# Kernel tuning notes

Hardware: AMD Instinct MI355X
Metric: run time of the kernel (lower is better)

Reference implementation:

```python
import jax, jax.numpy as jnp
import numpy as np

N, L, E, H = 2, 2048, 1024, 16
D = E // H  # head_dimension


def setup_inputs() -> dict:
    key = jax.random.key(0)
    kq, kk, kv, km, kw, kb = jax.random.split(key, 6)
    return {
        "query": jax.random.normal(kq, (N, L, E), dtype=jnp.float32),
        "key": jax.random.normal(kk, (N, L, E), dtype=jnp.float32),
        "value": jax.random.normal(kv, (N, L, E), dtype=jnp.float32),
        "mask": jax.random.randint(km, (N, 1, L, L), 0, 2, dtype=jnp.int32),
        "W_out": jax.random.normal(kw, (E, E), dtype=jnp.float32) / np.float32(np.sqrt(E)),
        "b_out": jax.random.normal(kb, (E,), dtype=jnp.float32) * np.float32(0.02),
    }


def reference(query, key, value, mask, W_out, b_out):
    n, ql, e = query.shape
    # split heads: [N, L, E] -> [N, L, H, D]
    q = query.reshape(n, ql, H, D)
    k = key.reshape(n, key.shape[1], H, D)
    v = value.reshape(n, value.shape[1], H, D)
    # energy: [N, H, Q, K]
    energy = jnp.einsum('nqhd,nkhd->nhqk', q, k)
    energy = jnp.where(mask == 0, jnp.float32(-1e20), energy)
    scale = jnp.float32(E) ** jnp.float32(0.5)
    attention = jax.nn.softmax(energy / scale, axis=3)
    out = jnp.einsum('nhql,nlhd->nqhd', attention, v).reshape(n, ql, H * D)
    # fully_connected_output: torch Linear -> x @ W^T + b
    return out @ W_out.T + b_out
```

## Files before the change

kernel.cpp:

```cpp
#include <hip/hip_runtime.h>
#include <hip/hip_bf16.h>

#define N_ 2
#define L_ 2048
#define E_ 1024
#define H_ 16
#define D_ 64

typedef __attribute__((ext_vector_type(8))) short bf16x8;
typedef __attribute__((ext_vector_type(4))) short bf16x4;
typedef __attribute__((ext_vector_type(4))) float f32x4;

static __device__ __forceinline__ short bfc(float f) {
    union { __bf16 h; short s; } u;
    u.h = (__bf16)f;
    return u.s;
}

static __device__ __forceinline__ void glds16(const void* g, void* l) {
    __builtin_amdgcn_global_load_lds(
        (const __attribute__((address_space(1))) unsigned int*)g,
        (__attribute__((address_space(3))) unsigned int*)l, 16, 0, 0);
}

__global__ __launch_bounds__(256) void pack_kv(
    const float* __restrict__ K, const float* __restrict__ V,
    unsigned short* __restrict__ Kp, unsigned short* __restrict__ Vp)
{
    __shared__ short T[64][72];

    const int bx = blockIdx.x;
    const int kt = bx & 31;
    const int h  = (bx >> 5) & 15;
    const int n  = bx >> 9;
    const int tid = threadIdx.x;
    const int kq = tid >> 4, c4 = tid & 15;

    const size_t inbase = ((size_t)(n * L_) + kt * 64) * E_ + h * D_;
    const size_t obase  = ((size_t)((n * H_ + h) * 32 + kt)) * 4096;

#pragma unroll
    for (int jj = 0; jj < 4; ++jj) {
        const int r = kq + jj * 16;
        const float4 f = *reinterpret_cast<const float4*>(K + inbase + (size_t)r * E_ + c4 * 4);
        bf16x4 w;
        w[0] = bfc(f.x); w[1] = bfc(f.y); w[2] = bfc(f.z); w[3] = bfc(f.w);
        *reinterpret_cast<bf16x4*>(&Kp[obase + r * 64 + ((c4 * 4) ^ ((r & 7) << 3))]) = w;
    }
#pragma unroll
    for (int jj = 0; jj < 4; ++jj) {
        const int k = kq + jj * 16;
        const float4 f = *reinterpret_cast<const float4*>(V + inbase + (size_t)k * E_ + c4 * 4);
        T[c4 * 4 + 0][k] = bfc(f.x);
        T[c4 * 4 + 1][k] = bfc(f.y);
        T[c4 * 4 + 2][k] = bfc(f.z);
        T[c4 * 4 + 3][k] = bfc(f.w);
    }
    __syncthreads();
#pragma unroll
    for (int jj = 0; jj < 2; ++jj) {
        const int d  = (tid >> 3) + jj * 32;
        const int k8 = (tid & 7) * 8;
        const bf16x8 v = *reinterpret_cast<const bf16x8*>(&T[d][k8]);
        *reinterpret_cast<bf16x8*>(&Vp[obase + d * 64 + (k8 ^ ((d & 7) << 3))]) = v;
    }
}

__global__ __launch_bounds__(256) void pack_mask(
    const int* __restrict__ mask, unsigned long long* __restrict__ Mb)
{
    const int tid  = threadIdx.x;
    const int lane = tid & 63;
    const int wave = tid >> 6;
    const int r = blockIdx.x * 4 + wave;
    const int* src = mask + (size_t)r * L_;
    unsigned long long* dst = Mb + (size_t)r * 32;
#pragma unroll 4
    for (int kt = 0; kt < 32; ++kt) {
        const int mv = src[kt * 64 + lane];
        const unsigned long long b = __ballot(mv != 0);
        if (lane == 0) dst[kt] = b;
    }
}

__global__ __launch_bounds__(256, 4) void attn_fwd(
    const unsigned short* __restrict__ Kp, const unsigned short* __restrict__ Vp,
    const float* __restrict__ Q, const unsigned long long* __restrict__ Mb,
    unsigned short* __restrict__ Obf )
{
    __shared__ __align__(16) short K_lds[2][64 * 64];
    __shared__ __align__(16) short V_lds[2][64 * 64];
    __shared__ __align__(16) short P_lds[4][16][64];

    const int tid   = threadIdx.x;
    const int lane  = tid & 63;
    const int wave  = tid >> 6;
    const int row16 = lane & 15;
    const int g     = lane >> 4;
    const int sw    = (row16 & 7) << 3;

    const int bid = blockIdx.x;
    const int bx  = (bid & 7) * 128 + (bid >> 3);
    const int qt = bx & 31;
    const int h  = (bx >> 5) & 15;
    const int n  = bx >> 9;

    const int q0w = qt * 64 + wave * 16;

    const float SCL = 0.0450842200277801f;

    const float* qptr = Q + ((size_t)(n * L_ + q0w + row16)) * E_ + h * D_;
    bf16x8 qa[2];
#pragma unroll
    for (int c = 0; c < 2; ++c) {
        const float4 f0 = *reinterpret_cast<const float4*>(qptr + 32 * c + 8 * g);
        const float4 f1 = *reinterpret_cast<const float4*>(qptr + 32 * c + 8 * g + 4);
        bf16x8 a;
        a[0] = bfc(f0.x * SCL); a[1] = bfc(f0.y * SCL);
        a[2] = bfc(f0.z * SCL); a[3] = bfc(f0.w * SCL);
        a[4] = bfc(f1.x * SCL); a[5] = bfc(f1.y * SCL);
        a[6] = bfc(f1.z * SCL); a[7] = bfc(f1.w * SCL);
        qa[c] = a;
    }

    f32x4 o[4];
#pragma unroll
    for (int dt = 0; dt < 4; ++dt) { o[dt][0] = 0.f; o[dt][1] = 0.f; o[dt][2] = 0.f; o[dt][3] = 0.f; }
    float lrun = 0.f;

    const unsigned long long* mrow = Mb + ((size_t)(n * L_) + q0w + row16) * 32;
    const char* kvb = (const char*)Kp + ((size_t)(n * H_ + h) * 32) * 8192;
    const char* vvb = (const char*)Vp + ((size_t)(n * H_ + h) * 32) * 8192;

    {
        const int off = wave * 2048;
        glds16(kvb + off + lane * 16,        (char*)&K_lds[0][0] + off);
        glds16(kvb + off + 1024 + lane * 16, (char*)&K_lds[0][0] + off + 1024);
        glds16(vvb + off + lane * 16,        (char*)&V_lds[0][0] + off);
        glds16(vvb + off + 1024 + lane * 16, (char*)&V_lds[0][0] + off + 1024);
    }
    __syncthreads();

    for (int kt = 0; kt < 32; ++kt) {
        const int cur = kt & 1;
        if (kt + 1 < 32) {
            const char* kg = kvb + (size_t)(kt + 1) * 8192;
            const char* vg = vvb + (size_t)(kt + 1) * 8192;
            const int off = wave * 2048;
            glds16(kg + off + lane * 16,        (char*)&K_lds[cur ^ 1][0] + off);
            glds16(kg + off + 1024 + lane * 16, (char*)&K_lds[cur ^ 1][0] + off + 1024);
            glds16(vg + off + lane * 16,        (char*)&V_lds[cur ^ 1][0] + off);
            glds16(vg + off + 1024 + lane * 16, (char*)&V_lds[cur ^ 1][0] + off + 1024);
        }
        const unsigned long long mb = mrow[kt];

        f32x4 s[4];
        __builtin_amdgcn_s_setprio(1);
#pragma unroll
        for (int t = 0; t < 4; ++t) {
            f32x4 acc; acc[0] = 0.f; acc[1] = 0.f; acc[2] = 0.f; acc[3] = 0.f;
#pragma unroll
            for (int c = 0; c < 2; ++c) {
                const bf16x8 kf = *reinterpret_cast<const bf16x8*>(
                    &K_lds[cur][(t * 16 + row16) * 64 + ((32 * c + 8 * g) ^ sw)]);
                acc = __builtin_amdgcn_mfma_f32_16x16x32_bf16(kf, qa[c], acc, 0, 0, 0);
            }
            s[t] = acc;
        }
        __builtin_amdgcn_s_setprio(0);

        const unsigned lo = (unsigned)(mb >> (g * 4));
        const unsigned hi = (unsigned)(mb >> (32 + g * 4));
        float ps = 0.f;
#pragma unroll
        for (int t = 0; t < 4; ++t) {
            const unsigned w32 = (t < 2) ? lo : hi;
            const int base = (t & 1) * 16;
#pragma unroll
            for (int i = 0; i < 4; ++i) {
                float p = exp2f(s[t][i]);
                p = (w32 & (1u << (base + i))) ? p : 0.0f;
                s[t][i] = p;
                ps += p;
            }
        }
        lrun += ps;

#pragma unroll
        for (int t = 0; t < 4; ++t) {
            bf16x4 w;
            w[0] = bfc(s[t][0]); w[1] = bfc(s[t][1]);
            w[2] = bfc(s[t][2]); w[3] = bfc(s[t][3]);
            *reinterpret_cast<bf16x4*>(
                &P_lds[wave][row16][(t * 16 + g * 4) ^ sw]) = w;
        }

        __builtin_amdgcn_s_setprio(1);
#pragma unroll
        for (int c = 0; c < 2; ++c) {
            const bf16x8 pb = *reinterpret_cast<const bf16x8*>(
                &P_lds[wave][row16][(32 * c + 8 * g) ^ sw]);
#pragma unroll
            for (int dt = 0; dt < 4; ++dt) {
                const bf16x8 va = *reinterpret_cast<const bf16x8*>(
                    &V_lds[cur][(dt * 16 + row16) * 64 + ((32 * c + 8 * g) ^ sw)]);
                o[dt] = __builtin_amdgcn_mfma_f32_16x16x32_bf16(va, pb, o[dt], 0, 0, 0);
            }
        }
        __builtin_amdgcn_s_setprio(0);

        __syncthreads();
    }

    float l = lrun;
    l += __shfl_xor(l, 16);
    l += __shfl_xor(l, 32);
    const float inv = 1.0f / l;
    unsigned short* ob = Obf + (size_t)(n * L_ + q0w + row16) * E_ + h * D_;
#pragma unroll
    for (int dt = 0; dt < 4; ++dt) {
        bf16x4 w;
        w[0] = bfc(o[dt][0] * inv); w[1] = bfc(o[dt][1] * inv);
        w[2] = bfc(o[dt][2] * inv); w[3] = bfc(o[dt][3] * inv);
        *reinterpret_cast<bf16x4*>(&ob[(dt * 16 + g * 4) ^ sw]) = w;
    }
}

__global__ __launch_bounds__(256) void attn_fwd_legacy(
    const unsigned short* __restrict__ Kp, const unsigned short* __restrict__ Vp,
    const float* __restrict__ Q, const int* __restrict__ mask,
    unsigned short* __restrict__ Obf)
{
    __shared__ __align__(16) short K_lds[64 * 64];
    __shared__ __align__(16) short V_lds[64 * 64];
    __shared__ __align__(16) short P_lds[4][16][64];

    const int tid   = threadIdx.x;
    const int lane  = tid & 63;
    const int wave  = tid >> 6;
    const int row16 = lane & 15;
    const int g     = lane >> 4;
    const int sw    = (row16 & 7) << 3;

    const int bx = blockIdx.x;
    const int qt = bx & 31;
    const int h  = (bx >> 5) & 15;
    const int n  = bx >> 9;

    const int q0w = qt * 64 + wave * 16;
    const float SCL = 0.0450842200277801f;

    const float* qptr = Q + ((size_t)(n * L_ + q0w + row16)) * E_ + h * D_;
    bf16x8 qa[2];
#pragma unroll
    for (int c = 0; c < 2; ++c) {
        const float4 f0 = *reinterpret_cast<const float4*>(qptr + 32 * c + 8 * g);
        const float4 f1 = *reinterpret_cast<const float4*>(qptr + 32 * c + 8 * g + 4);
        bf16x8 a;
        a[0] = bfc(f0.x * SCL); a[1] = bfc(f0.y * SCL);
        a[2] = bfc(f0.z * SCL); a[3] = bfc(f0.w * SCL);
        a[4] = bfc(f1.x * SCL); a[5] = bfc(f1.y * SCL);
        a[6] = bfc(f1.z * SCL); a[7] = bfc(f1.w * SCL);
        qa[c] = a;
    }

    f32x4 o[4];
#pragma unroll
    for (int dt = 0; dt < 4; ++dt) { o[dt][0] = 0.f; o[dt][1] = 0.f; o[dt][2] = 0.f; o[dt][3] = 0.f; }
    float lrun = 0.f;

    const int* mrow = mask + (size_t)n * L_ * L_ + (size_t)(q0w + row16) * L_;
    const char* kvb = (const char*)Kp + ((size_t)(n * H_ + h) * 32) * 8192;
    const char* vvb = (const char*)Vp + ((size_t)(n * H_ + h) * 32) * 8192;

    for (int kt = 0; kt < 32; ++kt) {
        int4 mv[4];
#pragma unroll
        for (int t = 0; t < 4; ++t)
            mv[t] = *reinterpret_cast<const int4*>(mrow + kt * 64 + t * 16 + g * 4);

        __syncthreads();
        {
            const char* kg = kvb + (size_t)kt * 8192;
            const char* vg = vvb + (size_t)kt * 8192;
#pragma unroll
            for (int it = 0; it < 2; ++it) {
                const int off = wave * 2048 + it * 1024;
                glds16(kg + off + lane * 16, (char*)K_lds + off);
                glds16(vg + off + lane * 16, (char*)V_lds + off);
            }
        }
        __syncthreads();

        f32x4 s[4];
#pragma unroll
        for (int t = 0; t < 4; ++t) {
            f32x4 acc; acc[0] = 0.f; acc[1] = 0.f; acc[2] = 0.f; acc[3] = 0.f;
#pragma unroll
            for (int c = 0; c < 2; ++c) {
                const bf16x8 kf = *reinterpret_cast<const bf16x8*>(
                    &K_lds[(t * 16 + row16) * 64 + ((32 * c + 8 * g) ^ sw)]);
                acc = __builtin_amdgcn_mfma_f32_16x16x32_bf16(kf, qa[c], acc, 0, 0, 0);
            }
            s[t] = acc;
        }
#pragma unroll
        for (int t = 0; t < 4; ++t) {
            s[t][0] = mv[t].x ? s[t][0] : -3.0e18f;
            s[t][1] = mv[t].y ? s[t][1] : -3.0e18f;
            s[t][2] = mv[t].z ? s[t][2] : -3.0e18f;
            s[t][3] = mv[t].w ? s[t][3] : -3.0e18f;
        }
        float ps = 0.f;
#pragma unroll
        for (int t = 0; t < 4; ++t) {
            const float p0 = exp2f(s[t][0]);
            const float p1 = exp2f(s[t][1]);
            const float p2 = exp2f(s[t][2]);
            const float p3 = exp2f(s[t][3]);
            s[t][0] = p0; s[t][1] = p1; s[t][2] = p2; s[t][3] = p3;
            ps += (p0 + p1) + (p2 + p3);
        }
        lrun += ps;
#pragma unroll
        for (int t = 0; t < 4; ++t) {
            bf16x4 w;
            w[0] = bfc(s[t][0]); w[1] = bfc(s[t][1]);
            w[2] = bfc(s[t][2]); w[3] = bfc(s[t][3]);
            *reinterpret_cast<bf16x4*>(&P_lds[wave][row16][(t * 16 + g * 4) ^ sw]) = w;
        }
#pragma unroll
        for (int c = 0; c < 2; ++c) {
            const bf16x8 pb = *reinterpret_cast<const bf16x8*>(
                &P_lds[wave][row16][(32 * c + 8 * g) ^ sw]);
#pragma unroll
            for (int dt = 0; dt < 4; ++dt) {
                const bf16x8 va = *reinterpret_cast<const bf16x8*>(
                    &V_lds[(dt * 16 + row16) * 64 + ((32 * c + 8 * g) ^ sw)]);
                o[dt] = __builtin_amdgcn_mfma_f32_16x16x32_bf16(va, pb, o[dt], 0, 0, 0);
            }
        }
    }

    float l = lrun;
    l += __shfl_xor(l, 16);
    l += __shfl_xor(l, 32);
    const float inv = 1.0f / l;
    unsigned short* ob = Obf + (size_t)(n * L_ + q0w + row16) * E_ + h * D_;
#pragma unroll
    for (int dt = 0; dt < 4; ++dt) {
        bf16x4 w;
        w[0] = bfc(o[dt][0] * inv); w[1] = bfc(o[dt][1] * inv);
        w[2] = bfc(o[dt][2] * inv); w[3] = bfc(o[dt][3] * inv);
        *reinterpret_cast<bf16x4*>(&ob[(dt * 16 + g * 4) ^ sw]) = w;
    }
}

__global__ __launch_bounds__(256) void convert_w(
    const float* __restrict__ W, unsigned short* __restrict__ Wb)
{
    const int i = (blockIdx.x * 256 + threadIdx.x) * 4;
    const int row = i >> 10, col = i & 1023;
    const float4 f = *reinterpret_cast<const float4*>(W + i);
    bf16x4 w;
    w[0] = bfc(f.x); w[1] = bfc(f.y); w[2] = bfc(f.z); w[3] = bfc(f.w);
    const int ch = col & ~63, incol = col & 63;
    *reinterpret_cast<bf16x4*>(&Wb[row * 1024 + ch + (incol ^ ((row & 7) << 3))]) = w;
}

__global__ __launch_bounds__(256, 4) void out_proj_bf(
    const unsigned short* __restrict__ A ,
    const unsigned short* __restrict__ Wb ,
    const float* __restrict__ bias, float* __restrict__ Cout)
{
    __shared__ __align__(16) short A_lds[2][128 * 64];
    __shared__ __align__(16) short W_lds[2][64 * 64];

    const int tid   = threadIdx.x;
    const int lane  = tid & 63;
    const int wave  = tid >> 6;
    const int row16 = lane & 15;
    const int g     = lane >> 4;
    const int sw    = (row16 & 7) << 3;

    const int bid = blockIdx.x;
    const int bx  = (bid & 7) * 64 + (bid >> 3);
    const int m0 = (bx & 31) * 128;
    const int n0 = (bx >> 5) * 64;

    const int ib = (lane & 7) * 16;
    const int rl = lane >> 3;

    f32x4 acc[2][4];
#pragma unroll
    for (int fm = 0; fm < 2; ++fm)
#pragma unroll
        for (int fn = 0; fn < 4; ++fn) {
            acc[fm][fn][0] = 0.f; acc[fm][fn][1] = 0.f;
            acc[fm][fn][2] = 0.f; acc[fm][fn][3] = 0.f;
        }

    {
#pragma unroll
        for (int it = 0; it < 4; ++it) {
            const int off = wave * 4096 + it * 1024;
            const int r = (off >> 7) + rl;
            glds16((const char*)A + (size_t)(m0 + r) * 2048 + ib, (char*)&A_lds[0][0] + off);
        }
#pragma unroll
        for (int it = 0; it < 2; ++it) {
            const int off = wave * 2048 + it * 1024;
            const int r = (off >> 7) + rl;
            glds16((const char*)Wb + (size_t)(n0 + r) * 2048 + ib, (char*)&W_lds[0][0] + off);
        }
    }
    __syncthreads();

    for (int kk = 0; kk < 16; ++kk) {
        const int cur = kk & 1;
        if (kk + 1 < 16) {
            const int kb = (kk + 1) * 128;
#pragma unroll
            for (int it = 0; it < 4; ++it) {
                const int off = wave * 4096 + it * 1024;
                const int r = (off >> 7) + rl;
                glds16((const char*)A + (size_t)(m0 + r) * 2048 + kb + ib,
                       (char*)&A_lds[cur ^ 1][0] + off);
            }
#pragma unroll
            for (int it = 0; it < 2; ++it) {
                const int off = wave * 2048 + it * 1024;
                const int r = (off >> 7) + rl;
                glds16((const char*)Wb + (size_t)(n0 + r) * 2048 + kb + ib,
                       (char*)&W_lds[cur ^ 1][0] + off);
            }
        }

        __builtin_amdgcn_s_setprio(1);
#pragma unroll
        for (int c = 0; c < 2; ++c) {
            bf16x8 af[2], wf[4];
#pragma unroll
            for (int fm = 0; fm < 2; ++fm)
                af[fm] = *reinterpret_cast<const bf16x8*>(
                    &A_lds[cur][(wave * 32 + fm * 16 + row16) * 64 + ((32 * c + 8 * g) ^ sw)]);
#pragma unroll
            for (int fn = 0; fn < 4; ++fn)
                wf[fn] = *reinterpret_cast<const bf16x8*>(
                    &W_lds[cur][(fn * 16 + row16) * 64 + ((32 * c + 8 * g) ^ sw)]);
#pragma unroll
            for (int fm = 0; fm < 2; ++fm)
#pragma unroll
                for (int fn = 0; fn < 4; ++fn)
                    acc[fm][fn] = __builtin_amdgcn_mfma_f32_16x16x32_bf16(
                        af[fm], wf[fn], acc[fm][fn], 0, 0, 0);
        }
        __builtin_amdgcn_s_setprio(0);

        __syncthreads();
    }

#pragma unroll
    for (int fm = 0; fm < 2; ++fm)
#pragma unroll
        for (int fn = 0; fn < 4; ++fn) {
            const int nn = n0 + fn * 16 + row16;
            const int mm = m0 + wave * 32 + fm * 16 + g * 4;
            const float b = bias[nn];
#pragma unroll
            for (int i = 0; i < 4; ++i)
                Cout[(size_t)(mm + i) * 1024 + nn] = acc[fm][fn][i] + b;
        }
}

__global__ __launch_bounds__(256) void out_proj_wf32(
    const unsigned short* __restrict__ A,
    const float* __restrict__ W,
    const float* __restrict__ bias, float* __restrict__ Cout)
{
    __shared__ __align__(16) short A_lds[128 * 64];
    __shared__ __align__(16) short W_lds[128 * 64];

    const int tid   = threadIdx.x;
    const int lane  = tid & 63;
    const int wave  = tid >> 6;
    const int row16 = lane & 15;
    const int g     = lane >> 4;
    const int sw    = (row16 & 7) << 3;
    const int wm = wave >> 1, wn = wave & 1;

    const int m0 = (blockIdx.x & 31) * 128;
    const int n0 = (blockIdx.x >> 5) * 128;

    f32x4 acc[4][4];
#pragma unroll
    for (int fm = 0; fm < 4; ++fm)
#pragma unroll
        for (int fn = 0; fn < 4; ++fn) {
            acc[fm][fn][0] = 0.f; acc[fm][fn][1] = 0.f;
            acc[fm][fn][2] = 0.f; acc[fm][fn][3] = 0.f;
        }

    for (int k0 = 0; k0 < 1024; k0 += 64) {
        __syncthreads();
#pragma unroll
        for (int it = 0; it < 4; ++it) {
            const int off = wave * 4096 + it * 1024;
            const int r = (off >> 7) + (lane >> 3);
            const int ib = (lane & 7) * 16;
            glds16((const char*)A + (size_t)(m0 + r) * 2048 + k0 * 2 + ib,
                   (char*)A_lds + off);
        }
#pragma unroll
        for (int it = 0; it < 2; ++it) {
            const int idx = tid + it * 256;
            const int r = idx >> 2, c16 = (idx & 3) * 16;
            const float* wp = W + (size_t)(n0 + r) * 1024 + k0 + c16;
            const float4 f0 = *reinterpret_cast<const float4*>(wp);
            const float4 f1 = *reinterpret_cast<const float4*>(wp + 4);
            const float4 f2 = *reinterpret_cast<const float4*>(wp + 8);
            const float4 f3 = *reinterpret_cast<const float4*>(wp + 12);
            bf16x8 w0, w1;
            w0[0] = bfc(f0.x); w0[1] = bfc(f0.y); w0[2] = bfc(f0.z); w0[3] = bfc(f0.w);
            w0[4] = bfc(f1.x); w0[5] = bfc(f1.y); w0[6] = bfc(f1.z); w0[7] = bfc(f1.w);
            w1[0] = bfc(f2.x); w1[1] = bfc(f2.y); w1[2] = bfc(f2.z); w1[3] = bfc(f2.w);
            w1[4] = bfc(f3.x); w1[5] = bfc(f3.y); w1[6] = bfc(f3.z); w1[7] = bfc(f3.w);
            const int swr = (r & 7) << 3;
            *reinterpret_cast<bf16x8*>(&W_lds[r * 64 + (c16 ^ swr)]) = w0;
            *reinterpret_cast<bf16x8*>(&W_lds[r * 64 + ((c16 + 8) ^ swr)]) = w1;
        }
        __syncthreads();

#pragma unroll
        for (int c = 0; c < 2; ++c) {
            bf16x8 af[4], wf[4];
#pragma unroll
            for (int f = 0; f < 4; ++f) {
                af[f] = *reinterpret_cast<const bf16x8*>(
                    &A_lds[(wm * 64 + f * 16 + row16) * 64 + ((32 * c + 8 * g) ^ sw)]);
                wf[f] = *reinterpret_cast<const bf16x8*>(
                    &W_lds[(wn * 64 + f * 16 + row16) * 64 + ((32 * c + 8 * g) ^ sw)]);
            }
#pragma unroll
            for (int fm = 0; fm < 4; ++fm)
#pragma unroll
                for (int fn = 0; fn < 4; ++fn)
                    acc[fm][fn] = __builtin_amdgcn_mfma_f32_16x16x32_bf16(
                        af[fm], wf[fn], acc[fm][fn], 0, 0, 0);
        }
    }

#pragma unroll
    for (int fm = 0; fm < 4; ++fm)
#pragma unroll
        for (int fn = 0; fn < 4; ++fn) {
            const int nn = n0 + wn * 64 + fn * 16 + row16;
            const int mm = m0 + wm * 64 + fm * 16 + g * 4;
            const float b = bias[nn];
#pragma unroll
            for (int i = 0; i < 4; ++i)
                Cout[(size_t)(mm + i) * 1024 + nn] = acc[fm][fn][i] + b;
        }
}

extern "C" void kernel_launch(void* const* d_in, const int* in_sizes, int n_in,
                              void* d_out, int out_size, void* d_ws, size_t ws_size,
                              hipStream_t stream) {
    const float* Q    = (const float*)d_in[0];
    const float* K    = (const float*)d_in[1];
    const float* V    = (const float*)d_in[2];
    const int*   mask = (const int*)d_in[3];
    const float* W    = (const float*)d_in[4];
    const float* b    = (const float*)d_in[5];
    float* out = (float*)d_out;

    unsigned short* Kp = (unsigned short*)d_out;
    unsigned short* Vp = (unsigned short*)d_out + (size_t)4096 * 1024;
    unsigned short* Ob = (unsigned short*)d_ws;

    const size_t MB1 = (size_t)1024 * 1024;

    pack_kv<<<dim3(1024), dim3(256), 0, stream>>>(K, V, Kp, Vp);

    if (ws_size >= 9 * MB1) {
        unsigned long long* Mbits = (unsigned long long*)((char*)d_ws + 8 * MB1);
        pack_mask<<<dim3(1024), dim3(256), 0, stream>>>(mask, Mbits);
        attn_fwd<<<dim3(1024), dim3(256), 0, stream>>>(Kp, Vp, Q, Mbits, Ob);
        if (ws_size >= 11 * MB1) {
            unsigned short* Wb = (unsigned short*)((char*)d_ws + 9 * MB1);
            convert_w<<<dim3(1024), dim3(256), 0, stream>>>(W, Wb);
            out_proj_bf<<<dim3(512), dim3(256), 0, stream>>>(Ob, Wb, b, out);
        } else {
            out_proj_wf32<<<dim3(256), dim3(256), 0, stream>>>(Ob, W, b, out);
        }
    } else {
        attn_fwd_legacy<<<dim3(1024), dim3(256), 0, stream>>>(Kp, Vp, Q, mask, Ob);
        if (ws_size >= 10 * MB1) {
            unsigned short* Wb = (unsigned short*)((char*)d_ws + 8 * MB1);
            convert_w<<<dim3(1024), dim3(256), 0, stream>>>(W, Wb);
            out_proj_bf<<<dim3(512), dim3(256), 0, stream>>>(Ob, Wb, b, out);
        } else {
            out_proj_wf32<<<dim3(256), dim3(256), 0, stream>>>(Ob, W, b, out);
        }
    }
}
```

Before: 226.3 us.

## Use 32x32 MFMA attention with two waves and fuse prep kernels

Replaces the 16x16 MFMA attention kernel with a 128-thread variant where each wave owns 32 query rows and uses 32x32x16 bf16 MFMAs for both QK^T and PV, cutting LDS fragment reads per flop. The separate K/V packing, mask bit-packing and weight conversion kernels are merged into one launch to remove launch overhead. Fewer waves per block may reduce latency hiding, and the wider accumulators raise register pressure.

Result: slower. 240.7 us (+6.4%).

```diff
diff --git a/kernel.cpp b/kernel.cpp
--- a/kernel.cpp
+++ b/kernel.cpp
@@ -10,6 +10,7 @@
 typedef __attribute__((ext_vector_type(8))) short bf16x8;
 typedef __attribute__((ext_vector_type(4))) short bf16x4;
 typedef __attribute__((ext_vector_type(4))) float f32x4;
+typedef __attribute__((ext_vector_type(16))) float f32x16;
 
 static __device__ __forceinline__ short bfc(float f) {
     union { __bf16 h; short s; } u;
@@ -21,6 +22,81 @@
     __builtin_amdgcn_global_load_lds(
         (const __attribute__((address_space(1))) unsigned int*)g,
         (__attribute__((address_space(3))) unsigned int*)l, 16, 0, 0);
+}
+
+__global__ __launch_bounds__(256) void prep_all(
+    const float* __restrict__ K, const float* __restrict__ V,
+    const int* __restrict__ mask, const float* __restrict__ W,
+    unsigned short* __restrict__ Kp, unsigned short* __restrict__ Vp,
+    unsigned long long* __restrict__ Mb, unsigned short* __restrict__ Wb)
+{
+    __shared__ short T[64][72];
+    const int b   = blockIdx.x;
+    const int tid = threadIdx.x;
+
+    if (b < 1024) {
+        const int kt = b & 31;
+        const int h  = (b >> 5) & 15;
+        const int n  = b >> 9;
+        const int kq = tid >> 4, c4 = tid & 15;
+
+        const size_t inbase = ((size_t)(n * L_) + kt * 64) * E_ + h * D_;
+        const size_t obase  = ((size_t)((n * H_ + h) * 32 + kt)) * 4096;
+
+#pragma unroll
+        for (int jj = 0; jj < 4; ++jj) {
+            const int r = kq + jj * 16;
+            const float4 f = *reinterpret_cast<const float4*>(K + inbase + (size_t)r * E_ + c4 * 4);
+            bf16x4 w;
+            w[0] = bfc(f.x); w[1] = bfc(f.y); w[2] = bfc(f.z); w[3] = bfc(f.w);
+            *reinterpret_cast<bf16x4*>(&Kp[obase + r * 64 + ((c4 * 4) ^ ((r & 7) << 3))]) = w;
+        }
+#pragma unroll
+        for (int jj = 0; jj < 4; ++jj) {
+            const int k = kq + jj * 16;
+            const float4 f = *reinterpret_cast<const float4*>(V + inbase + (size_t)k * E_ + c4 * 4);
+            T[c4 * 4 + 0][k] = bfc(f.x);
+            T[c4 * 4 + 1][k] = bfc(f.y);
+            T[c4 * 4 + 2][k] = bfc(f.z);
+            T[c4 * 4 + 3][k] = bfc(f.w);
+        }
+        __syncthreads();
+#pragma unroll
+        for (int jj = 0; jj < 2; ++jj) {
+            const int d  = (tid >> 3) + jj * 32;
+            const int k8 = (tid & 7) * 8;
+            const bf16x8 v = *reinterpret_cast<const bf16x8*>(&T[d][k8]);
+            *reinterpret_cast<bf16x8*>(&Vp[obase + d * 64 + (k8 ^ ((d & 7) << 3))]) = v;
+        }
+    } else if (b < 1536) {
+        const int lane = tid & 63;
+        const int wave = tid >> 6;
+        const int r0 = (b - 1024) * 8 + wave * 2;
+#pragma unroll
+        for (int rr = 0; rr < 2; ++rr) {
+            const int r = r0 + rr;
+            const int* src = mask + (size_t)r * L_;
+            unsigned long long* dst = Mb + (size_t)r * 32;
+#pragma unroll 4
+            for (int kt = 0; kt < 32; ++kt) {
+                const int mv = src[kt * 64 + lane];
+                const unsigned long long bl = __ballot(mv != 0);
+                if (lane == 0) dst[kt] = bl;
+            }
+        }
+    } else {
+        const int base = (b - 1536) * 4096;
+#pragma unroll
+        for (int j = 0; j < 4; ++j) {
+            const int i = base + (j * 256 + tid) * 4;
+            const int row = i >> 10, col = i & 1023;
+            const float4 f = *reinterpret_cast<const float4*>(W + i);
+            bf16x4 w;
+            w[0] = bfc(f.x); w[1] = bfc(f.y); w[2] = bfc(f.z); w[3] = bfc(f.w);
+            const int ch = col & ~63, incol = col & 63;
+            *reinterpret_cast<bf16x4*>(&Wb[row * 1024 + ch + (incol ^ ((row & 7) << 3))]) = w;
+        }
+    }
 }
 
 __global__ __launch_bounds__(256) void pack_kv(
@@ -28,7 +104,6 @@
     unsigned short* __restrict__ Kp, unsigned short* __restrict__ Vp)
 {
     __shared__ short T[64][72];
-
     const int bx = blockIdx.x;
     const int kt = bx & 31;
     const int h  = (bx >> 5) & 15;
@@ -83,13 +158,164 @@
     }
 }
 
-__global__ __launch_bounds__(256, 4) void attn_fwd(
+__global__ __launch_bounds__(128, 2) void attn_fwd32(
     const unsigned short* __restrict__ Kp, const unsigned short* __restrict__ Vp,
     const float* __restrict__ Q, const unsigned long long* __restrict__ Mb,
     unsigned short* __restrict__ Obf )
 {
     __shared__ __align__(16) short K_lds[2][64 * 64];
     __shared__ __align__(16) short V_lds[2][64 * 64];
+    __shared__ __align__(16) short P_lds[2][32][64];
+
+    const int tid  = threadIdx.x;
+    const int lane = tid & 63;
+    const int wave = tid >> 6;
+    const int q31  = lane & 31;
+    const int hi   = lane >> 5;
+    const int swl  = (lane & 7) << 3;
+
+    const int bid = blockIdx.x;
+    const int bx  = (bid & 7) * 128 + (bid >> 3);
+    const int qt = bx & 31;
+    const int h  = (bx >> 5) & 15;
+    const int n  = bx >> 9;
+
+    const int q0 = qt * 64 + wave * 32;
+
+    const float SCL = 0.0450842200277801f;
+
+    const float* qptr = Q + ((size_t)(n * L_ + q0 + q31)) * E_ + h * D_;
+    bf16x8 qa[4];
+#pragma unroll
+    for (int ds = 0; ds < 4; ++ds) {
+        const float4 f0 = *reinterpret_cast<const float4*>(qptr + ds * 16 + 8 * hi);
+        const float4 f1 = *reinterpret_cast<const float4*>(qptr + ds * 16 + 8 * hi + 4);
+        bf16x8 a;
+        a[0] = bfc(f0.x * SCL); a[1] = bfc(f0.y * SCL);
+        a[2] = bfc(f0.z * SCL); a[3] = bfc(f0.w * SCL);
+        a[4] = bfc(f1.x * SCL); a[5] = bfc(f1.y * SCL);
+        a[6] = bfc(f1.z * SCL); a[7] = bfc(f1.w * SCL);
+        qa[ds] = a;
+    }
+
+    f32x16 oacc[2];
+#pragma unroll
+    for (int dt = 0; dt < 2; ++dt)
+#pragma unroll
+        for (int r = 0; r < 16; ++r) oacc[dt][r] = 0.f;
+    float lrun = 0.f;
+
+    const unsigned long long* mrow = Mb + ((size_t)(n * L_) + q0 + q31) * 32;
+    const char* kvb = (const char*)Kp + ((size_t)(n * H_ + h) * 32) * 8192;
+    const char* vvb = (const char*)Vp + ((size_t)(n * H_ + h) * 32) * 8192;
+
+#pragma unroll
+    for (int it = 0; it < 4; ++it) {
+        const int off = wave * 4096 + it * 1024;
+        glds16(kvb + off + lane * 16, (char*)&K_lds[0][0] + off);
+        glds16(vvb + off + lane * 16, (char*)&V_lds[0][0] + off);
+    }
+    __syncthreads();
+
+    for (int kt = 0; kt < 32; ++kt) {
+        const int cur = kt & 1;
+        if (kt + 1 < 32) {
+            const char* kg = kvb + (size_t)(kt + 1) * 8192;
+            const char* vg = vvb + (size_t)(kt + 1) * 8192;
+#pragma unroll
+            for (int it = 0; it < 4; ++it) {
+                const int off = wave * 4096 + it * 1024;
+                glds16(kg + off + lane * 16, (char*)&K_lds[cur ^ 1][0] + off);
+                glds16(vg + off + lane * 16, (char*)&V_lds[cur ^ 1][0] + off);
+            }
+        }
+        const unsigned long long mb = mrow[kt];
+
+        f32x16 s0, s1;
+#pragma unroll
+        for (int r = 0; r < 16; ++r) { s0[r] = 0.f; s1[r] = 0.f; }
+        __builtin_amdgcn_s_setprio(1);
+#pragma unroll
+        for (int ds = 0; ds < 4; ++ds) {
+            const int col = (ds * 16 + 8 * hi) ^ swl;
+            const bf16x8 kf0 = *reinterpret_cast<const bf16x8*>(
+                &K_lds[cur][q31 * 64 + col]);
+            const bf16x8 kf1 = *reinterpret_cast<const bf16x8*>(
+                &K_lds[cur][(32 + q31) * 64 + col]);
+            s0 = __builtin_amdgcn_mfma_f32_32x32x16_bf16(kf0, qa[ds], s0, 0, 0, 0);
+            s1 = __builtin_amdgcn_mfma_f32_32x32x16_bf16(kf1, qa[ds], s1, 0, 0, 0);
+        }
+        __builtin_amdgcn_s_setprio(0);
+
+        const unsigned b0 = (unsigned)mb;
+        const unsigned b1 = (unsigned)(mb >> 32);
+        float ps = 0.f;
+#pragma unroll
+        for (int r = 0; r < 16; ++r) {
+            const int pos = (r & 3) + 8 * (r >> 2) + 4 * hi;
+            float p0 = exp2f(s0[r]);
+            p0 = (b0 & (1u << pos)) ? p0 : 0.f;
+            s0[r] = p0; ps += p0;
+            float p1 = exp2f(s1[r]);
+            p1 = (b1 & (1u << pos)) ? p1 : 0.f;
+            s1[r] = p1; ps += p1;
+        }
+        lrun += ps;
+
+#pragma unroll
+        for (int rg = 0; rg < 4; ++rg) {
+            bf16x4 w0, w1;
+#pragma unroll
+            for (int i = 0; i < 4; ++i) { w0[i] = bfc(s0[rg * 4 + i]); w1[i] = bfc(s1[rg * 4 + i]); }
+            *reinterpret_cast<bf16x4*>(
+                &P_lds[wave][q31][(rg * 8 + 4 * hi) ^ swl]) = w0;
+            *reinterpret_cast<bf16x4*>(
+                &P_lds[wave][q31][(32 + rg * 8 + 4 * hi) ^ swl]) = w1;
+        }
+
+        bf16x8 pf[4];
+#pragma unroll
+        for (int ks = 0; ks < 4; ++ks)
+            pf[ks] = *reinterpret_cast<const bf16x8*>(
+                &P_lds[wave][q31][(ks * 16 + 8 * hi) ^ swl]);
+        __builtin_amdgcn_s_setprio(1);
+#pragma unroll
+        for (int dt = 0; dt < 2; ++dt) {
+#pragma unroll
+            for (int ks = 0; ks < 4; ++ks) {
+                const bf16x8 va = *reinterpret_cast<const bf16x8*>(
+                    &V_lds[cur][(dt * 32 + q31) * 64 + ((ks * 16 + 8 * hi) ^ swl)]);
+                oacc[dt] = __builtin_amdgcn_mfma_f32_32x32x16_bf16(va, pf[ks], oacc[dt], 0, 0, 0);
+            }
+        }
+        __builtin_amdgcn_s_setprio(0);
+
+        __syncthreads();
+    }
+
+    const float l = lrun + __shfl_xor(lrun, 32);
+    const float inv = 1.0f / l;
+    unsigned short* ob = Obf + (size_t)(n * L_ + q0 + q31) * E_ + h * D_;
+#pragma unroll
+    for (int dt = 0; dt < 2; ++dt) {
+#pragma unroll
+        for (int rg = 0; rg < 4; ++rg) {
+            bf16x4 w;
+#pragma unroll
+            for (int i = 0; i < 4; ++i) w[i] = bfc(oacc[dt][rg * 4 + i] * inv);
+            *reinterpret_cast<bf16x4*>(
+                &ob[(dt * 32 + rg * 8 + 4 * hi) ^ swl]) = w;
+        }
+    }
+}
+
+__global__ __launch_bounds__(256) void attn_fwd_legacy(
+    const unsigned short* __restrict__ Kp, const unsigned short* __restrict__ Vp,
+    const float* __restrict__ Q, const int* __restrict__ mask,
+    unsigned short* __restrict__ Obf)
+{
+    __shared__ __align__(16) short K_lds[64 * 64];
+    __shared__ __align__(16) short V_lds[64 * 64];
     __shared__ __align__(16) short P_lds[4][16][64];
 
     const int tid   = threadIdx.x;
@@ -99,14 +325,12 @@
     const int g     = lane >> 4;
     const int sw    = (row16 & 7) << 3;
 
-    const int bid = blockIdx.x;
-    const int bx  = (bid & 7) * 128 + (bid >> 3);
+    const int bx = blockIdx.x;
     const int qt = bx & 31;
     const int h  = (bx >> 5) & 15;
     const int n  = bx >> 9;
 
     const int q0w = qt * 64 + wave * 16;
-
     const float SCL = 0.0450842200277801f;
 
     const float* qptr = Q + ((size_t)(n * L_ + q0w + row16)) * E_ + h * D_;
@@ -128,147 +352,6 @@
     for (int dt = 0; dt < 4; ++dt) { o[dt][0] = 0.f; o[dt][1] = 0.f; o[dt][2] = 0.f; o[dt][3] = 0.f; }
     float lrun = 0.f;
 
-    const unsigned long long* mrow = Mb + ((size_t)(n * L_) + q0w + row16) * 32;
-    const char* kvb = (const char*)Kp + ((size_t)(n * H_ + h) * 32) * 8192;
-    const char* vvb = (const char*)Vp + ((size_t)(n * H_ + h) * 32) * 8192;
-
-    {
-        const int off = wave * 2048;
-        glds16(kvb + off + lane * 16,        (char*)&K_lds[0][0] + off);
-        glds16(kvb + off + 1024 + lane * 16, (char*)&K_lds[0][0] + off + 1024);
-        glds16(vvb + off + lane * 16,        (char*)&V_lds[0][0] + off);
-        glds16(vvb + off + 1024 + lane * 16, (char*)&V_lds[0][0] + off + 1024);
-    }
-    __syncthreads();
-
-    for (int kt = 0; kt < 32; ++kt) {
-        const int cur = kt & 1;
-        if (kt + 1 < 32) {
-            const char* kg = kvb + (size_t)(kt + 1) * 8192;
-            const char* vg = vvb + (size_t)(kt + 1) * 8192;
-            const int off = wave * 2048;
-            glds16(kg + off + lane * 16,        (char*)&K_lds[cur ^ 1][0] + off);
-            glds16(kg + off + 1024 + lane * 16, (char*)&K_lds[cur ^ 1][0] + off + 1024);
-            glds16(vg + off + lane * 16,        (char*)&V_lds[cur ^ 1][0] + off);
-            glds16(vg + off + 1024 + lane * 16, (char*)&V_lds[cur ^ 1][0] + off + 1024);
-        }
-        const unsigned long long mb = mrow[kt];
-
-        f32x4 s[4];
-        __builtin_amdgcn_s_setprio(1);
-#pragma unroll
-        for (int t = 0; t < 4; ++t) {
-            f32x4 acc; acc[0] = 0.f; acc[1] = 0.f; acc[2] = 0.f; acc[3] = 0.f;
-#pragma unroll
-            for (int c = 0; c < 2; ++c) {
-                const bf16x8 kf = *reinterpret_cast<const bf16x8*>(
-                    &K_lds[cur][(t * 16 + row16) * 64 + ((32 * c + 8 * g) ^ sw)]);
-                acc = __builtin_amdgcn_mfma_f32_16x16x32_bf16(kf, qa[c], acc, 0, 0, 0);
-            }
-            s[t] = acc;
-        }
-        __builtin_amdgcn_s_setprio(0);
-
-        const unsigned lo = (unsigned)(mb >> (g * 4));
-        const unsigned hi = (unsigned)(mb >> (32 + g * 4));
-        float ps = 0.f;
-#pragma unroll
-        for (int t = 0; t < 4; ++t) {
-            const unsigned w32 = (t < 2) ? lo : hi;
-            const int base = (t & 1) * 16;
-#pragma unroll
-            for (int i = 0; i < 4; ++i) {
-                float p = exp2f(s[t][i]);
-                p = (w32 & (1u << (base + i))) ? p : 0.0f;
-                s[t][i] = p;
-                ps += p;
-            }
-        }
-        lrun += ps;
-
-#pragma unroll
-        for (int t = 0; t < 4; ++t) {
-            bf16x4 w;
-            w[0] = bfc(s[t][0]); w[1] = bfc(s[t][1]);
-            w[2] = bfc(s[t][2]); w[3] = bfc(s[t][3]);
-            *reinterpret_cast<bf16x4*>(
-                &P_lds[wave][row16][(t * 16 + g * 4) ^ sw]) = w;
-        }
-
-        __builtin_amdgcn_s_setprio(1);
-#pragma unroll
-        for (int c = 0; c < 2; ++c) {
-            const bf16x8 pb = *reinterpret_cast<const bf16x8*>(
-                &P_lds[wave][row16][(32 * c + 8 * g) ^ sw]);
-#pragma unroll
-            for (int dt = 0; dt < 4; ++dt) {
-                const bf16x8 va = *reinterpret_cast<const bf16x8*>(
-                    &V_lds[cur][(dt * 16 + row16) * 64 + ((32 * c + 8 * g) ^ sw)]);
-                o[dt] = __builtin_amdgcn_mfma_f32_16x16x32_bf16(va, pb, o[dt], 0, 0, 0);
-            }
-        }
-        __builtin_amdgcn_s_setprio(0);
-
-        __syncthreads();
-    }
-
-    float l = lrun;
-    l += __shfl_xor(l, 16);
-    l += __shfl_xor(l, 32);
-    const float inv = 1.0f / l;
-    unsigned short* ob = Obf + (size_t)(n * L_ + q0w + row16) * E_ + h * D_;
-#pragma unroll
-    for (int dt = 0; dt < 4; ++dt) {
-        bf16x4 w;
-        w[0] = bfc(o[dt][0] * inv); w[1] = bfc(o[dt][1] * inv);
-        w[2] = bfc(o[dt][2] * inv); w[3] = bfc(o[dt][3] * inv);
-        *reinterpret_cast<bf16x4*>(&ob[(dt * 16 + g * 4) ^ sw]) = w;
-    }
-}
-
-__global__ __launch_bounds__(256) void attn_fwd_legacy(
-    const unsigned short* __restrict__ Kp, const unsigned short* __restrict__ Vp,
-    const float* __restrict__ Q, const int* __restrict__ mask,
-    unsigned short* __restrict__ Obf)
-{
-    __shared__ __align__(16) short K_lds[64 * 64];
-    __shared__ __align__(16) short V_lds[64 * 64];
-    __shared__ __align__(16) short P_lds[4][16][64];
-
-    const int tid   = threadIdx.x;
-    const int lane  = tid & 63;
-    const int wave  = tid >> 6;
-    const int row16 = lane & 15;
-    const int g     = lane >> 4;
-    const int sw    = (row16 & 7) << 3;
-
-    const int bx = blockIdx.x;
-    const int qt = bx & 31;
-    const int h  = (bx >> 5) & 15;
-    const int n  = bx >> 9;
-
-    const int q0w = qt * 64 + wave * 16;
-    const float SCL = 0.0450842200277801f;
-
-    const float* qptr = Q + ((size_t)(n * L_ + q0w + row16)) * E_ + h * D_;
-    bf16x8 qa[2];
-#pragma unroll
-    for (int c = 0; c < 2; ++c) {
-        const float4 f0 = *reinterpret_cast<const float4*>(qptr + 32 * c + 8 * g);
-        const float4 f1 = *reinterpret_cast<const float4*>(qptr + 32 * c + 8 * g + 4);
-        bf16x8 a;
-        a[0] = bfc(f0.x * SCL); a[1] = bfc(f0.y * SCL);
-        a[2] = bfc(f0.z * SCL); a[3] = bfc(f0.w * SCL);
-        a[4] = bfc(f1.x * SCL); a[5] = bfc(f1.y * SCL);
-        a[6] = bfc(f1.z * SCL); a[7] = bfc(f1.w * SCL);
-        qa[c] = a;
-    }
-
-    f32x4 o[4];
-#pragma unroll
-    for (int dt = 0; dt < 4; ++dt) { o[dt][0] = 0.f; o[dt][1] = 0.f; o[dt][2] = 0.f; o[dt][3] = 0.f; }
-    float lrun = 0.f;
-
     const int* mrow = mask + (size_t)n * L_ * L_ + (size_t)(q0w + row16) * L_;
     const char* kvb = (const char*)Kp + ((size_t)(n * H_ + h) * 32) * 8192;
     const char* vvb = (const char*)Vp + ((size_t)(n * H_ + h) * 32) * 8192;
@@ -356,21 +439,9 @@
     }
 }
 
-__global__ __launch_bounds__(256) void convert_w(
-    const float* __restrict__ W, unsigned short* __restrict__ Wb)
-{
-    const int i = (blockIdx.x * 256 + threadIdx.x) * 4;
-    const int row = i >> 10, col = i & 1023;
-    const float4 f = *reinterpret_cast<const float4*>(W + i);
-    bf16x4 w;
-    w[0] = bfc(f.x); w[1] = bfc(f.y); w[2] = bfc(f.z); w[3] = bfc(f.w);
-    const int ch = col & ~63, incol = col & 63;
-    *reinterpret_cast<bf16x4*>(&Wb[row * 1024 + ch + (incol ^ ((row & 7) << 3))]) = w;
-}
-
 __global__ __launch_bounds__(256, 4) void out_proj_bf(
-    const unsigned short* __restrict__ A ,
-    const unsigned short* __restrict__ Wb ,
+    const unsigned short* __restrict__ A,
+    const unsigned short* __restrict__ Wb,
     const float* __restrict__ bias, float* __restrict__ Cout)
 {
     __shared__ __align__(16) short A_lds[2][128 * 64];
@@ -580,27 +651,21 @@
 
     const size_t MB1 = (size_t)1024 * 1024;
 
-    pack_kv<<<dim3(1024), dim3(256), 0, stream>>>(K, V, Kp, Vp);
-
-    if (ws_size >= 9 * MB1) {
+    if (ws_size >= 11 * MB1) {
         unsigned long long* Mbits = (unsigned long long*)((char*)d_ws + 8 * MB1);
+        unsigned short* Wb = (unsigned short*)((char*)d_ws + 9 * MB1);
+        prep_all<<<dim3(1792), dim3(256), 0, stream>>>(K, V, mask, W, Kp, Vp, Mbits, Wb);
+        attn_fwd32<<<dim3(1024), dim3(128), 0, stream>>>(Kp, Vp, Q, Mbits, Ob);
+        out_proj_bf<<<dim3(512), dim3(256), 0, stream>>>(Ob, Wb, b, out);
+    } else if (ws_size >= 9 * MB1) {
+        unsigned long long* Mbits = (unsigned long long*)((char*)d_ws + 8 * MB1);
+        pack_kv<<<dim3(1024), dim3(256), 0, stream>>>(K, V, Kp, Vp);
         pack_mask<<<dim3(1024), dim3(256), 0, stream>>>(mask, Mbits);
-        attn_fwd<<<dim3(1024), dim3(256), 0, stream>>>(Kp, Vp, Q, Mbits, Ob);
-        if (ws_size >= 11 * MB1) {
-            unsigned short* Wb = (unsigned short*)((char*)d_ws + 9 * MB1);
-            convert_w<<<dim3(1024), dim3(256), 0, stream>>>(W, Wb);
-            out_proj_bf<<<dim3(512), dim3(256), 0, stream>>>(Ob, Wb, b, out);
-        } else {
-            out_proj_wf32<<<dim3(256), dim3(256), 0, stream>>>(Ob, W, b, out);
-        }
+        attn_fwd32<<<dim3(1024), dim3(128), 0, stream>>>(Kp, Vp, Q, Mbits, Ob);
+        out_proj_wf32<<<dim3(256), dim3(256), 0, stream>>>(Ob, W, b, out);
     } else {
+        pack_kv<<<dim3(1024), dim3(256), 0, stream>>>(K, V, Kp, Vp);
         attn_fwd_legacy<<<dim3(1024), dim3(256), 0, stream>>>(Kp, Vp, Q, mask, Ob);
-        if (ws_size >= 10 * MB1) {
-            unsigned short* Wb = (unsigned short*)((char*)d_ws + 8 * MB1);
-            convert_w<<<dim3(1024), dim3(256), 0, stream>>>(W, Wb);
-            out_proj_bf<<<dim3(512), dim3(256), 0, stream>>>(Ob, Wb, b, out);
-        } else {
-            out_proj_wf32<<<dim3(256), dim3(256), 0, stream>>>(Ob, W, b, out);
-        }
-    }
-}
+        out_proj_wf32<<<dim3(256), dim3(256), 0, stream>>>(Ob, W, b, out);
+    }
+}
```
